# Performance work log

Measured on AMD Instinct MI355X. Metric: run time of the kernel, lower is better.

Reference implementation:

```python
import jax, jax.numpy as jnp
import numpy as np

TAU = 0.1

def setup_inputs() -> dict:
    key = jax.random.key(0)
    k1, k2 = jax.random.split(key)
    z_i = jax.random.normal(k1, (4096, 1024), dtype=jnp.float32)
    z_j = jax.random.normal(k2, (4096, 1024), dtype=jnp.float32)
    return {"z_i": z_i, "z_j": z_j}

def reference(z_i, z_j):
    N = z_i.shape[0]
    # L2-normalize each view (world_size=1 so gather is identity)
    k_i = z_i / jnp.linalg.norm(z_i, axis=-1, keepdims=True)
    k_j = z_j / jnp.linalg.norm(z_j, axis=-1, keepdims=True)
    k = jnp.concatenate([k_i, k_j], axis=0)          # [2N, D]
    # cosine similarity of normalized vectors == plain dot products
    sim = k @ k.T                                     # [2N, 2N]
    # positives: (i, i+N) and (i+N, i) pairs
    sim_ij = jnp.diagonal(sim, offset=N)
    sim_ji = jnp.diagonal(sim, offset=-N)
    positives = jnp.concatenate([sim_ij, sim_ji], axis=0)  # [2N]
    # denominator masks out self-similarity on the diagonal
    mask = ~jnp.eye(2 * N, dtype=bool)
    denom = jnp.sum(jnp.where(mask, jnp.exp(sim / TAU), 0.0), axis=1)  # [2N]
    all_losses = -(positives / TAU - jnp.log(denom))
    loss = jnp.sum(all_losses) / (2 * N)
    return loss
```

## Files before the change

### kernel.cpp

```cpp
#include <hip/hip_runtime.h>
#include <hip/hip_bf16.h>
#include <cstdint>
#include <math.h>

#define D_DIM 1024
#define TAU_INV 10.0f
#define EXP_SCALE (TAU_INV / 4096.0f)
#define BK 64
#define NT (D_DIM / BK)
#define BM 256
#define BN 128
#define SLOT 24576

typedef float f32x4 __attribute__((ext_vector_type(4)));

#define VMCNT(n) asm volatile("s_waitcnt vmcnt(" #n ")" ::: "memory")
#define LGKM0()  asm volatile("s_waitcnt lgkmcnt(0)" ::: "memory")
#define BAR() do { asm volatile("" ::: "memory"); \
                   __builtin_amdgcn_s_barrier();  \
                   asm volatile("" ::: "memory"); } while (0)

__device__ __forceinline__ float wave_reduce_add(float v) {
#pragma unroll
    for (int off = 32; off > 0; off >>= 1) v += __shfl_xor(v, off, 64);
    return v;
}

__global__ __launch_bounds__(256)
void norm_pos_kernel(const float* __restrict__ zi, const float* __restrict__ zj,
                     unsigned int* __restrict__ Kf, float* __restrict__ rowsum,
                     float* __restrict__ pos, int n_half) {
    const int i = blockIdx.x;
    const int t = threadIdx.x;
    float4 a = reinterpret_cast<const float4*>(zi + (size_t)i * D_DIM)[t];
    float4 b = reinterpret_cast<const float4*>(zj + (size_t)i * D_DIM)[t];
    float ssa = a.x*a.x + a.y*a.y + a.z*a.z + a.w*a.w;
    float ssb = b.x*b.x + b.y*b.y + b.z*b.z + b.w*b.w;
    float dab = a.x*b.x + a.y*b.y + a.z*b.z + a.w*b.w;
    ssa = wave_reduce_add(ssa);
    ssb = wave_reduce_add(ssb);
    dab = wave_reduce_add(dab);
    __shared__ float wsa[4], wsb[4], wsd[4];
    if ((t & 63) == 0) { wsa[t>>6] = ssa; wsb[t>>6] = ssb; wsd[t>>6] = dab; }
    __syncthreads();
    const float inva = 1.0f / sqrtf(wsa[0] + wsa[1] + wsa[2] + wsa[3]);
    const float invb = 1.0f / sqrtf(wsb[0] + wsb[1] + wsb[2] + wsb[3]);
    const float sa = inva * 64.0f;
    const float sb = invb * 64.0f;
    unsigned int ua = 0, ub = 0;
    ua = __builtin_amdgcn_cvt_pk_fp8_f32(a.x * sa, a.y * sa, ua, false);
    ua = __builtin_amdgcn_cvt_pk_fp8_f32(a.z * sa, a.w * sa, ua, true);
    ub = __builtin_amdgcn_cvt_pk_fp8_f32(b.x * sb, b.y * sb, ub, false);
    ub = __builtin_amdgcn_cvt_pk_fp8_f32(b.z * sb, b.w * sb, ub, true);
    Kf[(size_t)i * 256 + t] = ua;
    Kf[(size_t)(i + n_half) * 256 + t] = ub;
    if (t == 0) {
        pos[i] = (wsd[0] + wsd[1] + wsd[2] + wsd[3]) * inva * invb;
        rowsum[i] = 0.0f;
        rowsum[i + n_half] = 0.0f;
    }
}

__global__ __launch_bounds__(512, 4)
void simclr_gemm_kernel(const unsigned char* __restrict__ Kmat,
                        float* __restrict__ rowsum, int n_total) {
    __shared__ char lds[73728];

    const int tid  = threadIdx.x;
    const int lane = tid & 63;
    const int wave = tid >> 6;
    const int wr = wave >> 1;
    const int wc = wave & 1;
    const int kgrp = lane >> 4;

    const int wg = (blockIdx.x & 7) * 132 + (blockIdx.x >> 3);

    int by = 0, start = 0;
    while (wg >= start + (64 - 2 * by)) { start += 64 - 2 * by; ++by; }
    const int bx = 2 * by + (wg - start);
    const bool diag = ((bx >> 1) == by);
    const int rowbase = by * BM;
    const int colbase = bx * BN;

    const char* gK = reinterpret_cast<const char*>(Kmat);
    const int srow = tid >> 2;
    const int sswz = (tid & 3) ^ ((srow >> 1) & 3);

    auto stage_all = [&](int tt) {
        const int s = tt % 3;
        const size_t kbyte = (size_t)tt * BK;
        char* dstA = lds + s * SLOT + tid * 16;
        char* dstB = lds + s * SLOT + 16384 + tid * 16;
#pragma unroll
        for (int i = 0; i < 2; ++i) {
            const int row = i * 128 + srow;
            const char* src = gK + (size_t)(rowbase + row) * D_DIM + kbyte + sswz * 16;
            __builtin_amdgcn_global_load_lds(
                (const __attribute__((address_space(1))) void*)src,
                (__attribute__((address_space(3))) void*)(dstA + i * 8192),
                16, 0, 0);
        }
        {
            const char* src = gK + (size_t)(colbase + srow) * D_DIM + kbyte + sswz * 16;
            __builtin_amdgcn_global_load_lds(
                (const __attribute__((address_space(1))) void*)src,
                (__attribute__((address_space(3))) void*)dstB,
                16, 0, 0);
        }
    };

    f32x4 acc[4][4] = {};
    long af0[4], af1[4], bf0[4], bf1[4];

    auto read_half = [&](const char* base, int row, int h) -> long {
        const int xr = (row >> 1) & 3;
        const int s  = h * 2 + (kgrp >> 1);
        return *reinterpret_cast<const long*>(
            base + row * 64 + ((s ^ xr) << 4) + (kgrp & 1) * 8);
    };

    stage_all(0); stage_all(1);
    VMCNT(3); BAR();

    for (int t = 0; t < NT; ++t) {
        const int s = t % 3;
        const char* Ab = lds + s * SLOT;
        const char* Bb = Ab + 16384;
#pragma unroll
        for (int mi = 0; mi < 4; ++mi)
            af0[mi] = read_half(Ab, wr * 64 + mi * 16 + (lane & 15), 0);
#pragma unroll
        for (int ni = 0; ni < 4; ++ni)
            bf0[ni] = read_half(Bb, wc * 64 + ni * 16 + (lane & 15), 0);
#pragma unroll
        for (int mi = 0; mi < 4; ++mi)
            af1[mi] = read_half(Ab, wr * 64 + mi * 16 + (lane & 15), 1);
#pragma unroll
        for (int ni = 0; ni < 4; ++ni)
            bf1[ni] = read_half(Bb, wc * 64 + ni * 16 + (lane & 15), 1);
        if (t + 2 < NT) stage_all(t + 2);
        __builtin_amdgcn_s_setprio(1);
#pragma unroll
        for (int mi = 0; mi < 4; ++mi)
#pragma unroll
            for (int ni = 0; ni < 4; ++ni)
                acc[mi][ni] = __builtin_amdgcn_mfma_f32_16x16x32_fp8_fp8(
                    af0[mi], bf0[ni], acc[mi][ni], 0, 0, 0);
        __builtin_amdgcn_s_setprio(0);
        if (t < NT - 1) {
            LGKM0();
            if (t < NT - 2) { VMCNT(3); } else { VMCNT(0); }
            BAR();
        }
        __builtin_amdgcn_s_setprio(1);
#pragma unroll
        for (int mi = 0; mi < 4; ++mi)
#pragma unroll
            for (int ni = 0; ni < 4; ++ni)
                acc[mi][ni] = __builtin_amdgcn_mfma_f32_16x16x32_fp8_fp8(
                    af1[mi], bf1[ni], acc[mi][ni], 0, 0, 0);
        __builtin_amdgcn_s_setprio(0);
    }

    float colpart[4] = {0.0f, 0.0f, 0.0f, 0.0f};
#pragma unroll
    for (int mi = 0; mi < 4; ++mi) {
#pragma unroll
        for (int reg = 0; reg < 4; ++reg) {
            const int grow = rowbase + wr * 64 + mi * 16 + ((lane >> 4) << 2) + reg;
            float rowpart = 0.0f;
#pragma unroll
            for (int ni = 0; ni < 4; ++ni) {
                const int gcol = colbase + wc * 64 + ni * 16 + (lane & 15);
                float e = __expf(acc[mi][ni][reg] * EXP_SCALE);
                if (diag && grow == gcol) e = 0.0f;
                rowpart += e;
                colpart[ni] += e;
            }
#pragma unroll
            for (int off = 1; off < 16; off <<= 1)
                rowpart += __shfl_xor(rowpart, off, 64);
            if ((lane & 15) == 0) atomicAdd(&rowsum[grow], rowpart);
        }
    }
    if (!diag) {
#pragma unroll
        for (int ni = 0; ni < 4; ++ni) {
            float cp = colpart[ni];
            cp += __shfl_xor(cp, 16, 64);
            cp += __shfl_xor(cp, 32, 64);
            if (lane < 16)
                atomicAdd(&rowsum[colbase + wc * 64 + ni * 16 + lane], cp);
        }
    }
}

__global__ __launch_bounds__(256)
void loss_kernel(const float* __restrict__ rowsum, const float* __restrict__ pos,
                 float* __restrict__ out, int n_total, int n_half) {
    const int t = threadIdx.x;
    float acc = 0.0f;
    for (int r = t; r < n_total; r += 256) {
        const int pi = (r < n_half) ? r : (r - n_half);
        acc += logf(rowsum[r]) - TAU_INV * pos[pi];
    }
    acc = wave_reduce_add(acc);
    __shared__ float ws4[4];
    if ((t & 63) == 0) ws4[t >> 6] = acc;
    __syncthreads();
    if (t == 0) out[0] = (ws4[0] + ws4[1] + ws4[2] + ws4[3]) / (float)n_total;
}

extern "C" void kernel_launch(void* const* d_in, const int* in_sizes, int n_in,
                              void* d_out, int out_size, void* d_ws, size_t ws_size,
                              hipStream_t stream) {
    const float* zi = (const float*)d_in[0];
    const float* zj = (const float*)d_in[1];
    float* out = (float*)d_out;

    const int n_half  = in_sizes[0] / D_DIM;
    const int n_total = 2 * n_half;

    char* ws = (char*)d_ws;
    unsigned int* Kf = (unsigned int*)ws;
    size_t off = (size_t)n_total * D_DIM;
    float* rowsum = (float*)(ws + off); off += (size_t)n_total * 4;
    float* pos    = (float*)(ws + off); off += (size_t)n_half * 4;

    norm_pos_kernel<<<n_half, 256, 0, stream>>>(zi, zj, Kf, rowsum, pos, n_half);

    simclr_gemm_kernel<<<1056, 512, 0, stream>>>((const unsigned char*)Kf,
                                                 rowsum, n_total);

    loss_kernel<<<1, 256, 0, stream>>>(rowsum, pos, out, n_total, n_half);
}
```

Baseline: 88.53 us.

## Permute fp8 K layout so each lane reads both k-halves with one 128-bit LDS load

```diff
diff --git a/kernel.cpp b/kernel.cpp
--- a/kernel.cpp
+++ b/kernel.cpp
@@ -13,6 +13,7 @@
 #define SLOT 24576
 
 typedef float f32x4 __attribute__((ext_vector_type(4)));
+typedef long  l64x2 __attribute__((ext_vector_type(2)));
 
 #define VMCNT(n) asm volatile("s_waitcnt vmcnt(" #n ")" ::: "memory")
 #define LGKM0()  asm volatile("s_waitcnt lgkmcnt(0)" ::: "memory")
@@ -52,8 +53,9 @@
     ua = __builtin_amdgcn_cvt_pk_fp8_f32(a.z * sa, a.w * sa, ua, true);
     ub = __builtin_amdgcn_cvt_pk_fp8_f32(b.x * sb, b.y * sb, ub, false);
     ub = __builtin_amdgcn_cvt_pk_fp8_f32(b.z * sb, b.w * sb, ub, true);
-    Kf[(size_t)i * 256 + t] = ua;
-    Kf[(size_t)(i + n_half) * 256 + t] = ub;
+    const int w = (t >> 4) * 16 + ((t >> 1) & 3) * 4 + ((t >> 3) & 1) * 2 + (t & 1);
+    Kf[(size_t)i * 256 + w] = ua;
+    Kf[(size_t)(i + n_half) * 256 + w] = ub;
     if (t == 0) {
         pos[i] = (wsd[0] + wsd[1] + wsd[2] + wsd[3]) * inva * invb;
         rowsum[i] = 0.0f;
@@ -110,13 +112,11 @@
     };
 
     f32x4 acc[4][4] = {};
-    long af0[4], af1[4], bf0[4], bf1[4];
-
-    auto read_half = [&](const char* base, int row, int h) -> long {
-        const int xr = (row >> 1) & 3;
-        const int s  = h * 2 + (kgrp >> 1);
-        return *reinterpret_cast<const long*>(
-            base + row * 64 + ((s ^ xr) << 4) + (kgrp & 1) * 8);
+    l64x2 af[4], bf[4];
+
+    auto read_frag = [&](const char* base, int row) -> l64x2 {
+        return *reinterpret_cast<const l64x2*>(
+            base + row * 64 + ((kgrp ^ ((row >> 1) & 3)) << 4));
     };
 
     stage_all(0); stage_all(1);
@@ -128,16 +128,10 @@
         const char* Bb = Ab + 16384;
 #pragma unroll
         for (int mi = 0; mi < 4; ++mi)
-            af0[mi] = read_half(Ab, wr * 64 + mi * 16 + (lane & 15), 0);
+            af[mi] = read_frag(Ab, wr * 64 + mi * 16 + (lane & 15));
 #pragma unroll
         for (int ni = 0; ni < 4; ++ni)
-            bf0[ni] = read_half(Bb, wc * 64 + ni * 16 + (lane & 15), 0);
-#pragma unroll
-        for (int mi = 0; mi < 4; ++mi)
-            af1[mi] = read_half(Ab, wr * 64 + mi * 16 + (lane & 15), 1);
-#pragma unroll
-        for (int ni = 0; ni < 4; ++ni)
-            bf1[ni] = read_half(Bb, wc * 64 + ni * 16 + (lane & 15), 1);
+            bf[ni] = read_frag(Bb, wc * 64 + ni * 16 + (lane & 15));
         if (t + 2 < NT) stage_all(t + 2);
         __builtin_amdgcn_s_setprio(1);
 #pragma unroll
@@ -145,7 +139,7 @@
 #pragma unroll
             for (int ni = 0; ni < 4; ++ni)
                 acc[mi][ni] = __builtin_amdgcn_mfma_f32_16x16x32_fp8_fp8(
-                    af0[mi], bf0[ni], acc[mi][ni], 0, 0, 0);
+                    af[mi].x, bf[ni].x, acc[mi][ni], 0, 0, 0);
         __builtin_amdgcn_s_setprio(0);
         if (t < NT - 1) {
             LGKM0();
@@ -158,7 +152,7 @@
 #pragma unroll
             for (int ni = 0; ni < 4; ++ni)
                 acc[mi][ni] = __builtin_amdgcn_mfma_f32_16x16x32_fp8_fp8(
-                    af1[mi], bf1[ni], acc[mi][ni], 0, 0, 0);
+                    af[mi].y, bf[ni].y, acc[mi][ni], 0, 0, 0);
         __builtin_amdgcn_s_setprio(0);
     }
 
```

Result: faster. 82.07 us, median of 2 (-7.3%).
